# Performance work log

Measured on AMD Instinct MI355X. Metric: run time of the kernel, lower is better.

Reference implementation:

```python
import jax, jax.numpy as jnp
import numpy as np


def setup_inputs() -> dict:
    key = jax.random.key(0)
    k1, k2 = jax.random.split(key)
    pred = jax.random.normal(k1, (128, 1024), dtype=jnp.float32)
    y = jax.random.normal(k2, (128, 1024), dtype=jnp.float32)
    return {"pred": pred, "y": y}


def reference(pred, y):
    # Original: transpose to [N, C], then per-column soft Kendall tau.
    p = pred.T  # [N, C]
    l = y.T     # [N, C]
    n = p.shape[0]
    # Pairwise outer differences, batched across all C columns at once: [N, N, C]
    diff = p[:, None, :] - p[None, :, :]
    sgn = jnp.sign(l[:, None, :] - l[None, :, :])
    tmp = jnp.tanh(diff * sgn)
    # Diagonal entries are tanh(0) = 0, so subtracting the eye-masked diagonal
    # (as in the original) is a no-op; just sum everything.
    per_col = jnp.sum(tmp, axis=(0, 1)) / (n * (n - 1))  # [C]
    return 1.0 - per_col.mean()
```

## Files before the change

### kernel.cpp

```cpp
#include <hip/hip_runtime.h>


typedef float v2f __attribute__((ext_vector_type(2)));

#define TAU_N 1024
#define TAU_C 128
#define TILE  128
#define NTILE (TAU_N / TILE)
#define NTP   (NTILE * (NTILE + 1) / 2)
#define BPC   6
#define JOBS  (NTP / BPC)
#define PBLK  (TAU_C * BPC)
#define THR   512
#define IT    8

__device__ __constant__ unsigned char c_TI[NTP] = {
    0,1,1,2,2,2,3,3,3,3,4,4,4,4,4,5,5,5,5,5,5,
    6,6,6,6,6,6,6,7,7,7,7,7,7,7,7};
__device__ __constant__ unsigned char c_TJ[NTP] = {
    0,0,1,0,1,2,0,1,2,3,0,1,2,3,4,0,1,2,3,4,5,
    0,1,2,3,4,5,6,0,1,2,3,4,5,6,7};

__device__ __forceinline__ v2f tau_group(v2f m2, v2f mly, v2f t2, v2f l2, v2f acc) {
    const v2f one2 = {1.f, 1.f};
    v2f n  = m2 - t2;
    v2f d  = __builtin_elementwise_fma(-m2, t2, one2);
    v2f r  = {__builtin_amdgcn_rcpf(d.x), __builtin_amdgcn_rcpf(d.y)};
    v2f v  = n * r;
    v2f ld = mly - l2;
    v2f sv = {__uint_as_float(__float_as_uint(v.x) ^
                              (__float_as_uint(ld.x) & 0x80000000u)),
              __uint_as_float(__float_as_uint(v.y) ^
                              (__float_as_uint(ld.y) & 0x80000000u))};
    return acc + sv;
}

__global__ __launch_bounds__(THR, 6) void tau_tri_kernel(
        const float* __restrict__ pred, const float* __restrict__ y,
        float* __restrict__ out, float* __restrict__ acc_ws,
        unsigned* __restrict__ cnt_ws) {
    __shared__ __align__(16) float ts[TAU_N];
    __shared__ __align__(16) float ys[TAU_N];
    __shared__ float wsum[THR / 64];

    const int bx  = blockIdx.x;
    const int tid = threadIdx.x;
    const int c   = bx / BPC;
    const int jb0 = (bx % BPC) * JOBS;

    const float* p = pred + c * TAU_N;
    const float* l = y    + c * TAU_N;

    ts[tid]       = tanhf(p[tid]);
    ts[tid + THR] = tanhf(p[tid + THR]);
    ys[tid]       = l[tid];
    ys[tid + THR] = l[tid + THR];
    __syncthreads();

    const float4* t4 = (const float4*)ts;
    const float4* y4 = (const float4*)ys;
    const int ig = tid >> 5;
    const int js = tid & 31;

    float acc_tot = 0.f;

#pragma unroll
    for (int q = 0; q < JOBS; ++q) {
        const int job = jb0 + q;
        const int ti  = c_TI[job];
        const int tj  = c_TJ[job];

        const int ib4 = (ti * TILE + ig * IT) >> 2;
        const float4 ta = t4[ib4], tb = t4[ib4 + 1];
        const float4 la = y4[ib4], lb = y4[ib4 + 1];
        const float mt[IT] = {ta.x, ta.y, ta.z, ta.w, tb.x, tb.y, tb.z, tb.w};
        const float ml[IT] = {la.x, la.y, la.z, la.w, lb.x, lb.y, lb.z, lb.w};

        const int jb4 = (tj * TILE + js * 4) >> 2;
        const float4 tj4 = t4[jb4];
        const float4 yj4 = y4[jb4];
        const v2f tA = {tj4.x, tj4.y}, tB = {tj4.z, tj4.w};
        const v2f lA = {yj4.x, yj4.y}, lB = {yj4.z, yj4.w};

        v2f a0 = {0.f,0.f}, a1 = {0.f,0.f}, a2 = {0.f,0.f}, a3 = {0.f,0.f};
#pragma unroll
        for (int a = 0; a < IT; ++a) {
            const v2f m2  = {mt[a], mt[a]};
            const v2f mly = {ml[a], ml[a]};
            if (a & 1) {
                a1 = tau_group(m2, mly, tA, lA, a1);
                a3 = tau_group(m2, mly, tB, lB, a3);
            } else {
                a0 = tau_group(m2, mly, tA, lA, a0);
                a2 = tau_group(m2, mly, tB, lB, a2);
            }
        }
        const v2f asum = (a0 + a1) + (a2 + a3);
        const float s = asum.x + asum.y;
        acc_tot += (ti == tj) ? 0.5f * s : s;
    }

    for (int off = 32; off >= 1; off >>= 1)
        acc_tot += __shfl_down(acc_tot, off, 64);
    if ((tid & 63) == 0) wsum[tid >> 6] = acc_tot;
    __syncthreads();
    if (tid == 0) {
        float t = 0.f;
#pragma unroll
        for (int w = 0; w < THR / 64; ++w) t += wsum[w];
        atomicAdd(acc_ws, t);
        __threadfence();
        unsigned old = atomicAdd(cnt_ws, 1u);
        if (old == PBLK - 1) {
            __threadfence();
            float total = atomicAdd(acc_ws, 0.0f);
            const float scale = 2.0f / ((float)TAU_N * (float)(TAU_N - 1) * (float)TAU_C);
            out[0] = 1.0f - total * scale;
        }
    }
}

extern "C" void kernel_launch(void* const* d_in, const int* in_sizes, int n_in,
                              void* d_out, int out_size, void* d_ws, size_t ws_size,
                              hipStream_t stream) {
    const float* pred = (const float*)d_in[0];
    const float* y    = (const float*)d_in[1];
    float* out        = (float*)d_out;
    float* acc_ws     = (float*)d_ws;
    unsigned* cnt_ws  = (unsigned*)d_ws + 1;

    hipMemsetAsync(d_ws, 0, 2 * sizeof(unsigned), stream);
    tau_tri_kernel<<<PBLK, THR, 0, stream>>>(pred, y, out, acc_ws, cnt_ws);
}
```

Before: 80.56 us.

## Use 1024-thread blocks, fuse sign into FMA, two-kernel deterministic reduction

Changes the work split to 4 blocks per column with 1024 threads each, so every thread handles 4 rows instead of 8. The tanh-difference product is folded into an FMA by applying the sign to the numerator, and the diagonal half-weight now comes from a constant table. The atomic counter reduction and its memset are replaced by per-block partials and a separate single-block finalize kernel. This removes atomics and the memset launch but adds a second kernel launch, and halving per-thread work lowers ILP while adding more per-thread load overhead.

```diff
diff --git a/kernel.cpp b/kernel.cpp
--- a/kernel.cpp
+++ b/kernel.cpp
@@ -8,11 +8,11 @@
 #define TILE  128
 #define NTILE (TAU_N / TILE)
 #define NTP   (NTILE * (NTILE + 1) / 2)
-#define BPC   6
+#define BPC   4
 #define JOBS  (NTP / BPC)
 #define PBLK  (TAU_C * BPC)
-#define THR   512
-#define IT    8
+#define THR   1024
+#define IT    4
 
 __device__ __constant__ unsigned char c_TI[NTP] = {
     0,1,1,2,2,2,3,3,3,3,4,4,4,4,4,5,5,5,5,5,5,
@@ -20,41 +20,40 @@
 __device__ __constant__ unsigned char c_TJ[NTP] = {
     0,0,1,0,1,2,0,1,2,3,0,1,2,3,4,0,1,2,3,4,5,
     0,1,2,3,4,5,6,0,1,2,3,4,5,6,7};
+__device__ __constant__ float c_W[NTP] = {
+    0.5f,1,0.5f,1,1,0.5f,1,1,1,0.5f,1,1,1,1,0.5f,1,1,1,1,1,0.5f,
+    1,1,1,1,1,1,0.5f,1,1,1,1,1,1,1,0.5f};
 
 __device__ __forceinline__ v2f tau_group(v2f m2, v2f mly, v2f t2, v2f l2, v2f acc) {
     const v2f one2 = {1.f, 1.f};
     v2f n  = m2 - t2;
     v2f d  = __builtin_elementwise_fma(-m2, t2, one2);
     v2f r  = {__builtin_amdgcn_rcpf(d.x), __builtin_amdgcn_rcpf(d.y)};
-    v2f v  = n * r;
     v2f ld = mly - l2;
-    v2f sv = {__uint_as_float(__float_as_uint(v.x) ^
+    v2f ns = {__uint_as_float(__float_as_uint(n.x) ^
                               (__float_as_uint(ld.x) & 0x80000000u)),
-              __uint_as_float(__float_as_uint(v.y) ^
+              __uint_as_float(__float_as_uint(n.y) ^
                               (__float_as_uint(ld.y) & 0x80000000u))};
-    return acc + sv;
+    return __builtin_elementwise_fma(ns, r, acc);
 }
 
-__global__ __launch_bounds__(THR, 6) void tau_tri_kernel(
+__global__ __launch_bounds__(THR, 8) void tau_tri_kernel(
         const float* __restrict__ pred, const float* __restrict__ y,
-        float* __restrict__ out, float* __restrict__ acc_ws,
-        unsigned* __restrict__ cnt_ws) {
+        float* __restrict__ partials) {
     __shared__ __align__(16) float ts[TAU_N];
     __shared__ __align__(16) float ys[TAU_N];
     __shared__ float wsum[THR / 64];
 
     const int bx  = blockIdx.x;
     const int tid = threadIdx.x;
-    const int c   = bx / BPC;
-    const int jb0 = (bx % BPC) * JOBS;
+    const int c   = bx >> 2;
+    const int jb0 = (bx & (BPC - 1)) * JOBS;
 
     const float* p = pred + c * TAU_N;
     const float* l = y    + c * TAU_N;
 
-    ts[tid]       = tanhf(p[tid]);
-    ts[tid + THR] = tanhf(p[tid + THR]);
-    ys[tid]       = l[tid];
-    ys[tid + THR] = l[tid + THR];
+    ts[tid] = tanhf(p[tid]);
+    ys[tid] = l[tid];
     __syncthreads();
 
     const float4* t4 = (const float4*)ts;
@@ -69,18 +68,17 @@
         const int job = jb0 + q;
         const int ti  = c_TI[job];
         const int tj  = c_TJ[job];
+        const float w = c_W[job];
 
-        const int ib4 = (ti * TILE + ig * IT) >> 2;
-        const float4 ta = t4[ib4], tb = t4[ib4 + 1];
-        const float4 la = y4[ib4], lb = y4[ib4 + 1];
-        const float mt[IT] = {ta.x, ta.y, ta.z, ta.w, tb.x, tb.y, tb.z, tb.w};
-        const float ml[IT] = {la.x, la.y, la.z, la.w, lb.x, lb.y, lb.z, lb.w};
+        const float4 mt4 = t4[ti * (TILE / 4) + ig];
+        const float4 ml4 = y4[ti * (TILE / 4) + ig];
+        const float4 tj4 = t4[tj * (TILE / 4) + js];
+        const float4 yj4 = y4[tj * (TILE / 4) + js];
 
-        const int jb4 = (tj * TILE + js * 4) >> 2;
-        const float4 tj4 = t4[jb4];
-        const float4 yj4 = y4[jb4];
         const v2f tA = {tj4.x, tj4.y}, tB = {tj4.z, tj4.w};
         const v2f lA = {yj4.x, yj4.y}, lB = {yj4.z, yj4.w};
+        const float mt[IT] = {mt4.x, mt4.y, mt4.z, mt4.w};
+        const float ml[IT] = {ml4.x, ml4.y, ml4.z, ml4.w};
 
         v2f a0 = {0.f,0.f}, a1 = {0.f,0.f}, a2 = {0.f,0.f}, a3 = {0.f,0.f};
 #pragma unroll
@@ -96,8 +94,7 @@
             }
         }
         const v2f asum = (a0 + a1) + (a2 + a3);
-        const float s = asum.x + asum.y;
-        acc_tot += (ti == tj) ? 0.5f * s : s;
+        acc_tot = __builtin_fmaf(w, asum.x + asum.y, acc_tot);
     }
 
     for (int off = 32; off >= 1; off >>= 1)
@@ -108,15 +105,25 @@
         float t = 0.f;
 #pragma unroll
         for (int w = 0; w < THR / 64; ++w) t += wsum[w];
-        atomicAdd(acc_ws, t);
-        __threadfence();
-        unsigned old = atomicAdd(cnt_ws, 1u);
-        if (old == PBLK - 1) {
-            __threadfence();
-            float total = atomicAdd(acc_ws, 0.0f);
-            const float scale = 2.0f / ((float)TAU_N * (float)(TAU_N - 1) * (float)TAU_C);
-            out[0] = 1.0f - total * scale;
-        }
+        partials[bx] = t;
+    }
+}
+
+__global__ __launch_bounds__(PBLK) void tau_finalize_kernel(
+        const float* __restrict__ partials, float* __restrict__ out) {
+    __shared__ float wsum[PBLK / 64];
+    const int tid = threadIdx.x;
+    float acc = partials[tid];
+    for (int off = 32; off >= 1; off >>= 1)
+        acc += __shfl_down(acc, off, 64);
+    if ((tid & 63) == 0) wsum[tid >> 6] = acc;
+    __syncthreads();
+    if (tid == 0) {
+        float t = 0.f;
+#pragma unroll
+        for (int w = 0; w < PBLK / 64; ++w) t += wsum[w];
+        const float scale = 2.0f / ((float)TAU_N * (float)(TAU_N - 1) * (float)TAU_C);
+        out[0] = 1.0f - t * scale;
     }
 }
 
@@ -126,9 +133,8 @@
     const float* pred = (const float*)d_in[0];
     const float* y    = (const float*)d_in[1];
     float* out        = (float*)d_out;
-    float* acc_ws     = (float*)d_ws;
-    unsigned* cnt_ws  = (unsigned*)d_ws + 1;
+    float* partials   = (float*)d_ws;
 
-    hipMemsetAsync(d_ws, 0, 2 * sizeof(unsigned), stream);
-    tau_tri_kernel<<<PBLK, THR, 0, stream>>>(pred, y, out, acc_ws, cnt_ws);
+    tau_tri_kernel<<<PBLK, THR, 0, stream>>>(pred, y, partials);
+    tau_finalize_kernel<<<1, PBLK, 0, stream>>>(partials, out);
 }
```

Result: faster. 69.84 us (-13.3%).
